# Kernel tuning notes

Measured on AMD Instinct MI355X. Metric: run time of the kernel, lower is better.

Reference implementation:

```python
import jax, jax.numpy as jnp
import numpy as np

B, S, D = 2, 2048, 1024
H, HD = 16, 64
HIDDEN = 2730  # int(1024 * 4 * 2/3)
WINDOW = 512
EPS = 1e-6


def rmsnorm(x, w):
    return x * jax.lax.rsqrt(jnp.mean(x * x, axis=-1, keepdims=True) + EPS) * w


def rope(q, k):
    # q, k: [B, H, S, HD]; half-split rotate_half convention, base 10000
    inv_freq = 1.0 / (10000.0 ** (jnp.arange(0, HD, 2, dtype=jnp.float32) / HD))
    pos = jnp.arange(S, dtype=jnp.float32)
    freqs = pos[:, None] * inv_freq[None, :]          # [S, HD/2]
    cos = jnp.concatenate([jnp.cos(freqs)] * 2, -1)    # [S, HD]
    sin = jnp.concatenate([jnp.sin(freqs)] * 2, -1)

    def rot_half(x):
        x1, x2 = jnp.split(x, 2, axis=-1)
        return jnp.concatenate([-x2, x1], axis=-1)

    q = q * cos + rot_half(q) * sin
    k = k * cos + rot_half(k) * sin
    return q, k


def setup_inputs() -> dict:
    key = jax.random.key(0)
    ks = jax.random.split(key, 6)
    return {
        "x": jax.random.normal(ks[0], (B, S, D), jnp.float32),
        "norm1_w": jnp.ones((D,), jnp.float32),
        "norm2_w": jnp.ones((D,), jnp.float32),
        "w_qkv": jax.random.normal(ks[1], (3 * D, D), jnp.float32) * 0.02,
        "qnorm_w": jnp.ones((HD,), jnp.float32),
        "knorm_w": jnp.ones((HD,), jnp.float32),
        "w_o": jax.random.normal(ks[2], (D, D), jnp.float32) * (0.02 / 2 ** 0.5),
        "w1": jax.random.normal(ks[3], (HIDDEN, D), jnp.float32) * 0.02,
        "w3": jax.random.normal(ks[4], (HIDDEN, D), jnp.float32) * 0.02,
        "w2": jax.random.normal(ks[5], (D, HIDDEN), jnp.float32) * 0.02,
    }


def reference(x, norm1_w, norm2_w, w_qkv, qnorm_w, knorm_w, w_o, w1, w3, w2):
    h = rmsnorm(x, norm1_w)                              # [B,S,D]
    qkv = jnp.einsum("bsd,ed->bse", h, w_qkv)            # [B,S,3D]
    q, k, v = jnp.split(qkv, 3, axis=-1)

    def heads(t):  # [B,S,D] -> [B,H,S,HD]
        return t.reshape(B, S, H, HD).transpose(0, 2, 1, 3)

    q, k, v = heads(q), heads(k), heads(v)
    q = rmsnorm(q, qnorm_w)  # qk_norm over head_dim
    k = rmsnorm(k, knorm_w)
    q, k = rope(q, k)

    scale = HD ** -0.5
    scores = jnp.einsum("bhqd,bhkd->bhqk", q, k) * scale  # [B,H,S,S]
    pos = jnp.arange(S)
    row, col = pos[:, None], pos[None, :]
    masked = (col > row) | (col < row - WINDOW + 1)       # True = don't attend
    scores = jnp.where(masked[None, None], -jnp.inf, scores)
    attn = jax.nn.softmax(scores, axis=-1)
    out = jnp.einsum("bhqk,bhkd->bhqd", attn, v)          # [B,H,S,HD]
    out = out.transpose(0, 2, 1, 3).reshape(B, S, D)
    out = jnp.einsum("bsd,ed->bse", out, w_o)

    x = x + out
    h2 = rmsnorm(x, norm2_w)
    gate = jax.nn.silu(jnp.einsum("bsd,hd->bsh", h2, w1))
    up = jnp.einsum("bsd,hd->bsh", h2, w3)
    ffn = jnp.einsum("bsh,dh->bsd", gate * up, w2)
    return x + ffn
```

## Files before the change

### kernel.cpp

```cpp
#include <hip/hip_runtime.h>

typedef unsigned short u16;
typedef unsigned int   u32;
typedef __bf16 bf16x8 __attribute__((ext_vector_type(8)));
typedef __bf16 bf16x2 __attribute__((ext_vector_type(2)));
typedef float  f32x4  __attribute__((ext_vector_type(4)));
typedef float  f32x2  __attribute__((ext_vector_type(2)));

#define DEV static __device__ __forceinline__
#define NEG_INF (-__builtin_inff())

DEV u16 f2bf(float f) {
  u32 u = __builtin_bit_cast(u32, f);
  u += 0x7fffu + ((u >> 16) & 1u);
  return (u16)(u >> 16);
}

DEV float bf2f(u16 v) {
  u32 u = (u32)v << 16;
  return __builtin_bit_cast(float, u);
}

DEV u32 packbf(float a, float b) {
  f32x2 v = {a, b};
  bf16x2 r = __builtin_convertvector(v, bf16x2);
  return __builtin_bit_cast(u32, r);
}

typedef __attribute__((address_space(1))) void gvoid_t;
typedef __attribute__((address_space(3))) void svoid_t;

DEV void async16(const void* g, void* l) {
  __builtin_amdgcn_global_load_lds((gvoid_t*)g, (svoid_t*)l, 16, 0, 0);
}

DEV f32x4 mfma_bf16(bf16x8 a, bf16x8 b, f32x4 c) {
  return __builtin_amdgcn_mfma_f32_16x16x32_bf16(a, b, c, 0, 0, 0);
}

#define SBAR() __builtin_amdgcn_sched_barrier(0)
#define BARRIER() do { SBAR(); __builtin_amdgcn_s_barrier(); SBAR(); } while (0)
#define LGK0() do { asm volatile("s_waitcnt lgkmcnt(0)" ::: "memory"); SBAR(); } while (0)
#define VMC(n) do { asm volatile("s_waitcnt vmcnt(" #n ")" ::: "memory"); SBAR(); } while (0)

__global__ void cvt_bf16_k(const float* __restrict__ s, u16* __restrict__ d, int n4) {
  int i = blockIdx.x * blockDim.x + threadIdx.x;
  if (i >= n4) return;
  float4 v = ((const float4*)s)[i];
  ((ushort4*)d)[i] = make_ushort4(f2bf(v.x), f2bf(v.y), f2bf(v.z), f2bf(v.w));
}

__global__ void w13_prep_k(const float* __restrict__ w1, const float* __restrict__ w3,
                           u16* __restrict__ d, int n4) {
  int i = blockIdx.x * blockDim.x + threadIdx.x;
  if (i >= n4) return;
  int e = i * 4;
  int r = e >> 10;
  int c = e & 1023;
  int blk = r >> 4, j = r & 15;
  int srow = (blk >> 1) * 16 + j;
  ushort4 o = make_ushort4(0, 0, 0, 0);
  if (srow < 2730) {
    const float* src = (blk & 1) ? w3 : w1;
    float4 v = *(const float4*)&src[(size_t)srow * 1024 + c];
    o = make_ushort4(f2bf(v.x), f2bf(v.y), f2bf(v.z), f2bf(v.w));
  }
  ((ushort4*)d)[i] = o;
}

__global__ void pad_cols_k(const float* __restrict__ s, u16* __restrict__ d,
                           int Cs, int Cd, int n4) {
  int i = blockIdx.x * blockDim.x + threadIdx.x;
  if (i >= n4) return;
  int e = i * 4;
  int r = e / Cd;
  int c = e - r * Cd;
  u16 o[4];
#pragma unroll
  for (int j = 0; j < 4; ++j) {
    int cc = c + j;
    o[j] = (cc < Cs) ? f2bf(s[(size_t)r * Cs + cc]) : (u16)0;
  }
  ((ushort4*)d)[i] = make_ushort4(o[0], o[1], o[2], o[3]);
}

__global__ void rmsnorm_cvt_k(const float* __restrict__ in, const float* __restrict__ w,
                              u16* __restrict__ out) {
  __shared__ float red[4];
  int row = blockIdx.x;
  int t = threadIdx.x;
  const float4 v = ((const float4*)(in + (size_t)row * 1024))[t];
  float ss = v.x * v.x + v.y * v.y + v.z * v.z + v.w * v.w;
#pragma unroll
  for (int off = 1; off < 64; off <<= 1) ss += __shfl_xor(ss, off);
  if ((t & 63) == 0) red[t >> 6] = ss;
  __syncthreads();
  float tot = red[0] + red[1] + red[2] + red[3];
  float rs = rsqrtf(tot * (1.0f / 1024.0f) + 1e-6f);
  const float4 wv = ((const float4*)w)[t];
  ((ushort4*)(out + (size_t)row * 1024))[t] =
      make_ushort4(f2bf(v.x * rs * wv.x), f2bf(v.y * rs * wv.y),
                   f2bf(v.z * rs * wv.z), f2bf(v.w * rs * wv.w));
}

__global__ void qk_post_k(const u16* __restrict__ qkv, const float* __restrict__ qw,
                          const float* __restrict__ kw, u16* __restrict__ Qb,
                          u16* __restrict__ Kb) {
  int g = blockIdx.x * 4 + (threadIdx.x >> 6);
  int d = threadIdx.x & 63;
  int b = g >> 15;
  int r = g & 32767;
  int s = r >> 4;
  int h = r & 15;
  size_t base = ((size_t)(b * 2048 + s)) * 3072 + h * 64 + d;
  float qv = bf2f(qkv[base]);
  float kv = bf2f(qkv[base + 1024]);
  float q2 = qv * qv, k2 = kv * kv;
#pragma unroll
  for (int off = 1; off < 64; off <<= 1) {
    q2 += __shfl_xor(q2, off);
    k2 += __shfl_xor(k2, off);
  }
  float qn = qv * rsqrtf(q2 * (1.0f / 64.0f) + 1e-6f) * qw[d];
  float kn = kv * rsqrtf(k2 * (1.0f / 64.0f) + 1e-6f) * kw[d];
  int j = d & 31;
  float invf = __expf((float)j * -0.28782313662425572f);
  float ang = (float)s * invf;
  float sn, cs;
  sincosf(ang, &sn, &cs);
  float pq = __shfl_xor(qn, 32);
  float pk = __shfl_xor(kn, 32);
  float qo = (d < 32) ? (qn * cs - pq * sn) : (qn * cs + pq * sn);
  float ko = (d < 32) ? (kn * cs - pk * sn) : (kn * cs + pk * sn);
  size_t ob = ((size_t)((b * 16 + h) * 2048 + s)) * 64 + d;
  Qb[ob] = f2bf(qo);
  Kb[ob] = f2bf(ko);
}

__global__ void vtrans_k(const u16* __restrict__ qkv, u16* __restrict__ VT) {
  __shared__ u16 tile[64][65];
  int bh = blockIdx.y;
  int b = bh >> 4, h = bh & 15;
  int s0 = blockIdx.x * 64;
  int t = threadIdx.x;
  int tx = t & 63, ty = t >> 6;
#pragma unroll
  for (int p = 0; p < 16; ++p) {
    int sl = p * 4 + ty;
    tile[sl][tx] = qkv[((size_t)(b * 2048 + s0 + sl)) * 3072 + 2048 + h * 64 + tx];
  }
  __syncthreads();
#pragma unroll
  for (int p = 0; p < 16; ++p) {
    int dl = p * 4 + ty;
    VT[((size_t)(bh * 64 + dl)) * 2048 + s0 + tx] = tile[tx][dl];
  }
}

template <int EPI>
__global__ __launch_bounds__(256, 1) void gemm128p(
    const u16* __restrict__ A, const u16* __restrict__ B0,
    const float* __restrict__ res, void* __restrict__ outp, int M, int N, int K, int NT) {
  __shared__ u16 S[49152];
  const int tid = threadIdx.x;
  const int lane = tid & 63;
  const int wv = tid >> 6;
  const int wr = wv >> 1;
  const int wc = wv & 1;
  const int c16 = lane & 15, g4 = lane >> 4;

  const int gx = gridDim.x;
  const int nwg = gx * gridDim.y;
  const int lin = blockIdx.x + gx * blockIdx.y;
  const int swz = (lin & 7) * (nwg >> 3) + (lin >> 3);
  const int bm = (swz / gx) * 128;
  const int bn = (swz % gx) * 128;

  const int strow = tid >> 3;
  const int stcs = ((tid & 7) ^ (strow & 7)) * 8;
  const u16* Ap = A + (size_t)(bm + strow) * K + stcs;
  const u16* Bp = B0 + (size_t)(bn + strow) * K + stcs;
  const int wvb = wv * 512;

#define STG(bufi, t) do { const size_t _o = (size_t)(t) * 64; _Pragma("unroll") \
    for (int s = 0; s < 4; ++s) { \
      async16(Ap + _o + (size_t)s * 32 * K, &S[(bufi) * 16384 + s * 2048 + wvb]); \
      async16(Bp + _o + (size_t)s * 32 * K, &S[(bufi) * 16384 + 8192 + s * 2048 + wvb]); \
    } } while (0)

  f32x4 acc[4][4] = {};
  const int xk0 = (g4 ^ (c16 & 7)) * 8;
  const int xk1 = ((4 + g4) ^ (c16 & 7)) * 8;
  const int arb = (wr * 64 + c16) * 64;
  const int brb = 8192 + (wc * 64 + c16) * 64;

  STG(0, 0);
  STG(1, 1);
  VMC(8); BARRIER();

  int cur = 0;
  for (int kt = 0; kt < NT; ++kt) {
    int n2 = cur + 2; if (n2 >= 3) n2 -= 3;
    if (kt + 2 < NT) {
      if (n2 == 0) STG(0, kt + 2);
      else if (n2 == 1) STG(1, kt + 2);
      else STG(2, kt + 2);
    }
    bf16x8 a[4][2], b[4][2];
    const int cb = cur * 16384;
#pragma unroll
    for (int mf = 0; mf < 4; ++mf) {
      a[mf][0] = *(const bf16x8*)&S[cb + arb + mf * 1024 + xk0];
      a[mf][1] = *(const bf16x8*)&S[cb + arb + mf * 1024 + xk1];
    }
#pragma unroll
    for (int nf = 0; nf < 4; ++nf) {
      b[nf][0] = *(const bf16x8*)&S[cb + brb + nf * 1024 + xk0];
      b[nf][1] = *(const bf16x8*)&S[cb + brb + nf * 1024 + xk1];
    }
    LGK0();
    __builtin_amdgcn_s_setprio(1);
#pragma unroll
    for (int ks = 0; ks < 2; ++ks)
#pragma unroll
      for (int mf = 0; mf < 4; ++mf)
#pragma unroll
        for (int nf = 0; nf < 4; ++nf)
          acc[mf][nf] = mfma_bf16(a[mf][ks], b[nf][ks], acc[mf][nf]);
    __builtin_amdgcn_s_setprio(0);
    if (kt + 2 < NT) { VMC(8); } else { VMC(0); }
    BARRIER();
    cur = cur + 1; if (cur >= 3) cur = 0;
  }

#pragma unroll
  for (int mf = 0; mf < 4; ++mf)
#pragma unroll
    for (int nf = 0; nf < 4; ++nf) {
      int row = bm + wr * 64 + mf * 16 + g4 * 4;
      int col = bn + wc * 64 + nf * 16 + c16;
#pragma unroll
      for (int r = 0; r < 4; ++r) {
        size_t idx = (size_t)(row + r) * (size_t)N + col;
        if constexpr (EPI == 1) {
          ((float*)outp)[idx] = res[idx] + acc[mf][nf][r];
        } else {
          ((u16*)outp)[idx] = f2bf(acc[mf][nf][r]);
        }
      }
    }
#undef STG
}

template <int QM, int QN>
DEV void mmq(f32x4 (&acc)[8][4], const bf16x8 (&a)[4][2], const bf16x8 (&b)[2][2]) {
#pragma unroll
  for (int mf = 0; mf < 4; ++mf)
#pragma unroll
    for (int nf = 0; nf < 2; ++nf) {
      acc[QM * 4 + mf][QN * 2 + nf] = mfma_bf16(a[mf][0], b[nf][0], acc[QM * 4 + mf][QN * 2 + nf]);
      acc[QM * 4 + mf][QN * 2 + nf] = mfma_bf16(a[mf][1], b[nf][1], acc[QM * 4 + mf][QN * 2 + nf]);
    }
}

template <int EPI>
__global__ __launch_bounds__(512, 2) void gemm256(
    const u16* __restrict__ A, const u16* __restrict__ B0,
    void* __restrict__ outp, int M, int N, int K, int NT) {
  __shared__ u16 S[65536];
  const int tid = threadIdx.x;
  const int lane = tid & 63;
  const int wv = tid >> 6;
  const int wr = wv >> 2;
  const int wc = wv & 3;
  const int c16 = lane & 15, g4 = lane >> 4;

  int gx = gridDim.x;
  int nwg = gx * gridDim.y;
  int lin = blockIdx.x + gx * blockIdx.y;
  int swz = ((nwg & 7) == 0) ? ((lin & 7) * (nwg >> 3) + (lin >> 3)) : lin;
  const int bm = (swz / gx) * 256;
  const int bn = (swz % gx) * 256;

  const int sr = tid >> 2;
  const int sc2s = ((tid & 3) * 16) ^ (((sr >> 3) & 1) << 5);
  const int scol = sc2s >> 1;
  const u16* Asrc = A + (size_t)(bm + sr) * K + scol;
  const u16* Bsrc = B0 + (size_t)(bn + sr) * K + scol;
  const int ldst = wv * 512;

#define STA(buf, h, t) do { \
    const u16* _g = Asrc + (size_t)(h) * 128 * K + (t) * 64; \
    async16(_g,      &S[(buf) * 16384 + (h) * 8192 + ldst]); \
    async16(_g + 32, &S[(buf) * 16384 + (h) * 8192 + 4096 + ldst]); } while (0)
#define STB(buf, h, t) do { \
    const u16* _g = Bsrc + (size_t)(h) * 128 * K + (t) * 64; \
    async16(_g,      &S[32768 + (buf) * 16384 + (h) * 8192 + ldst]); \
    async16(_g + 32, &S[32768 + (buf) * 16384 + (h) * 8192 + 4096 + ldst]); } while (0)

  const int xr = (g4 * 8) ^ (((c16 >> 3) & 1) << 4);
  const int raOff = c16 * 32 + xr;
  const int abase0 = wr * 8192;
  const int bbase0 = 32768 + (wc >> 1) * 8192 + (wc & 1) * 2048;

#define LDA(buf, qm) do { _Pragma("unroll") \
    for (int mf = 0; mf < 4; ++mf) { \
      int _ro = (buf) * 16384 + abase0 + ((qm) * 64 + mf * 16) * 32 + raOff; \
      a[mf][0] = *(const bf16x8*)&S[_ro]; \
      a[mf][1] = *(const bf16x8*)&S[_ro + 4096]; } } while (0)
#define LDB(buf, qn, bq) do { _Pragma("unroll") \
    for (int nf = 0; nf < 2; ++nf) { \
      int _ro = (buf) * 16384 + bbase0 + ((qn) * 2 + nf) * 512 + raOff; \
      bq[nf][0] = *(const bf16x8*)&S[_ro]; \
      bq[nf][1] = *(const bf16x8*)&S[_ro + 4096]; } } while (0)

  f32x4 acc[8][4] = {};
  bf16x8 a[4][2], bq0[2][2], bq1[2][2];

  STB(0, 0, 0); STA(0, 0, 0); STB(0, 1, 0); STA(0, 1, 0);
  STB(1, 0, 1); STA(1, 0, 1);
  VMC(4); BARRIER();

  for (int kt = 0; kt < NT; ++kt) {
    const int buf = kt & 1, ob = buf ^ 1;
    const int t1 = (kt + 1 < NT) ? kt + 1 : NT - 1;
    const int t2 = (kt + 2 < NT) ? kt + 2 : NT - 1;
    LDA(buf, 0); LDB(buf, 0, bq0);
    STB(ob, 1, t1);
    BARRIER(); LGK0();
    __builtin_amdgcn_s_setprio(1); mmq<0, 0>(acc, a, bq0); __builtin_amdgcn_s_setprio(0);
    BARRIER();
    LDB(buf, 1, bq1);
    STA(ob, 1, t1);
    BARRIER(); LGK0();
    __builtin_amdgcn_s_setprio(1); mmq<0, 1>(acc, a, bq1); __builtin_amdgcn_s_setprio(0);
    BARRIER();
    LDA(buf, 1);
    STB(buf, 0, t2);
    BARRIER(); LGK0();
    __builtin_amdgcn_s_setprio(1); mmq<1, 0>(acc, a, bq0); __builtin_amdgcn_s_setprio(0);
    BARRIER();
    STA(buf, 0, t2);
    BARRIER();
    __builtin_amdgcn_s_setprio(1); mmq<1, 1>(acc, a, bq1); __builtin_amdgcn_s_setprio(0);
    VMC(4); BARRIER();
  }
  asm volatile("s_waitcnt vmcnt(0)" ::: "memory");

#pragma unroll
  for (int mf = 0; mf < 8; ++mf) {
    int row0 = bm + wr * 128 + mf * 16 + g4 * 4;
    if constexpr (EPI == 0) {
#pragma unroll
      for (int nf = 0; nf < 4; ++nf) {
        int col = bn + wc * 64 + nf * 16 + c16;
#pragma unroll
        for (int r = 0; r < 4; ++r)
          ((float*)outp)[(size_t)(row0 + r) * N + col] = acc[mf][nf][r];
      }
    } else {
      const int NH = N >> 1;
#pragma unroll
      for (int p = 0; p < 2; ++p) {
        int hid = ((bn + wc * 64) >> 1) + p * 16 + c16;
#pragma unroll
        for (int r = 0; r < 4; ++r) {
          float gg = acc[mf][2 * p][r];
          float uu = acc[mf][2 * p + 1][r];
          ((u16*)outp)[(size_t)(row0 + r) * NH + hid] = f2bf(gg * uu / (1.0f + __expf(-gg)));
        }
      }
    }
  }
#undef STA
#undef STB
#undef LDA
#undef LDB
}

__global__ __launch_bounds__(256, 4) void attn_k(const u16* __restrict__ Q,
                                                 const u16* __restrict__ Kb,
                                                 const u16* __restrict__ VT,
                                                 u16* __restrict__ O) {
  __shared__ u16 KT[2 * 2048];
  __shared__ u16 VTl[2 * 2048];
  __shared__ float bsm[4][16];
  __shared__ u16 Plds[4][16 * 40];
  const int tid = threadIdx.x;
  const int lane = tid & 63;
  const int wv = tid >> 6;
  const int bh = blockIdx.y;
  const int q0b = blockIdx.x * 64;
  const int q0 = q0b + wv * 16;
  const int c16 = lane & 15;
  const int hi = lane >> 4;
  const u16* Qp = Q + ((size_t)bh * 2048 + q0) * 64;

  const bf16x8 qf0 = *(const bf16x8*)&Qp[c16 * 64 + hi * 8];
  const bf16x8 qf1 = *(const bf16x8*)&Qp[c16 * 64 + 32 + hi * 8];

  const int krow = tid >> 3;
  const int kcs = ((tid & 7) ^ (krow & 7)) * 8;
  const u16* Ksrc = Kb + (size_t)bh * 131072 + (size_t)krow * 64 + kcs;
  const int vrow = tid >> 2;
  const int vcs = ((tid & 3) ^ ((vrow >> 1) & 3)) * 8;
  const u16* Vsrc = VT + (size_t)bh * 131072 + (size_t)vrow * 2048 + vcs;
  const int wvb = wv * 512;

  f32x4 o[4] = {};
  float m = -30.0f;
  float psum = 0.0f;
  const float SCL = 0.125f * 1.4426950408889634f;
  int startb = q0b - 511;
  if (startb < 0) startb = 0;
  startb &= ~31;
  const int kgend = q0b + 32;
  u16* Pw = Plds[wv];
  float* bw = bsm[wv];

  const int xh0 = (hi ^ (c16 & 7)) * 8;
  const int xh4 = ((4 + hi) ^ (c16 & 7)) * 8;
  const int xv = (hi ^ ((c16 >> 1) & 3)) * 8;

  async16(Ksrc + (size_t)startb * 64, &KT[wvb]);
  async16(Vsrc + startb, &VTl[wvb]);

  int buf = 0;
  for (int kg = startb; kg <= kgend; kg += 32) {
    if (kg + 32 <= kgend) {
      async16(Ksrc + (size_t)(kg + 32) * 64, &KT[(buf ^ 1) * 2048 + wvb]);
      async16(Vsrc + (kg + 32), &VTl[(buf ^ 1) * 2048 + wvb]);
      VMC(2);
    } else {
      VMC(0);
    }
    BARRIER();
    if (kg <= q0 + 15 && kg >= q0 - 542) {
      const int kb = buf * 2048 + c16 * 64;
      bf16x8 k00 = *(const bf16x8*)&KT[kb + xh0];
      bf16x8 k01 = *(const bf16x8*)&KT[kb + xh4];
      bf16x8 k10 = *(const bf16x8*)&KT[kb + 1024 + xh0];
      bf16x8 k11 = *(const bf16x8*)&KT[kb + 1024 + xh4];
      bf16x8 vf[4];
#pragma unroll
      for (int n = 0; n < 4; ++n)
        vf[n] = *(const bf16x8*)&VTl[buf * 2048 + (n * 16 + c16) * 32 + xv];
      LGK0();

      f32x4 slo = {0.f, 0.f, 0.f, 0.f}, shi2 = {0.f, 0.f, 0.f, 0.f};
      __builtin_amdgcn_s_setprio(1);
      slo = mfma_bf16(k00, qf0, slo);
      slo = mfma_bf16(k01, qf1, slo);
      shi2 = mfma_bf16(k10, qf0, shi2);
      shi2 = mfma_bf16(k11, qf1, shi2);
      __builtin_amdgcn_s_setprio(0);

      float sc[8];
#pragma unroll
      for (int r = 0; r < 4; ++r) {
        sc[r] = slo[r] * SCL;
        sc[4 + r] = shi2[r] * SCL;
      }
      const bool inter = (kg + 31 <= q0) && (kg >= q0 - 496);
      if (!inter) {
        const int row = q0 + c16;
#pragma unroll
        for (int r = 0; r < 4; ++r) {
          int col = kg + hi * 4 + r;
          if (!(col <= row && col > row - 512)) sc[r] = -1e30f;
          int col2 = col + 16;
          if (!(col2 <= row && col2 > row - 512)) sc[4 + r] = -1e30f;
        }
      }
      float tmax = fmaxf(fmaxf(fmaxf(sc[0], sc[1]), fmaxf(sc[2], sc[3])),
                         fmaxf(fmaxf(sc[4], sc[5]), fmaxf(sc[6], sc[7])));
      tmax = fmaxf(tmax, __shfl_xor(tmax, 16));
      tmax = fmaxf(tmax, __shfl_xor(tmax, 32));
      if (__any(tmax > m + 8.0f)) {
        float mn = fmaxf(m, tmax);
        float corr = exp2f(m - mn);
        m = mn;
        psum *= corr;
        bw[c16] = corr;
        __builtin_amdgcn_wave_barrier();
        float cr[4];
#pragma unroll
        for (int r = 0; r < 4; ++r) cr[r] = bw[hi * 4 + r];
        __builtin_amdgcn_wave_barrier();
#pragma unroll
        for (int n = 0; n < 4; ++n)
#pragma unroll
          for (int r = 0; r < 4; ++r) o[n][r] *= cr[r];
      }
      float p[8];
#pragma unroll
      for (int i = 0; i < 8; ++i) p[i] = exp2f(sc[i] - m);
      psum += ((p[0] + p[1]) + (p[2] + p[3])) + ((p[4] + p[5]) + (p[6] + p[7]));

      uint2 wlo, whi2;
      wlo.x = packbf(p[0], p[1]);
      wlo.y = packbf(p[2], p[3]);
      whi2.x = packbf(p[4], p[5]);
      whi2.y = packbf(p[6], p[7]);
      *(uint2*)&Pw[c16 * 40 + hi * 4] = wlo;
      *(uint2*)&Pw[c16 * 40 + 16 + hi * 4] = whi2;
      __builtin_amdgcn_wave_barrier();
      bf16x8 pa = *(const bf16x8*)&Pw[c16 * 40 + hi * 8];
      __builtin_amdgcn_wave_barrier();
      __builtin_amdgcn_s_setprio(1);
#pragma unroll
      for (int n = 0; n < 4; ++n) o[n] = mfma_bf16(pa, vf[n], o[n]);
      __builtin_amdgcn_s_setprio(0);
    }
    BARRIER();
    buf ^= 1;
  }

  psum += __shfl_xor(psum, 16);
  psum += __shfl_xor(psum, 32);
  bw[c16] = psum;
  __builtin_amdgcn_wave_barrier();
  const int b = bh >> 4, h = bh & 15;
#pragma unroll
  for (int r = 0; r < 4; ++r) {
    float inv = 1.0f / bw[hi * 4 + r];
    int row = q0 + hi * 4 + r;
#pragma unroll
    for (int n = 0; n < 4; ++n)
      O[((size_t)(b * 2048 + row)) * 1024 + h * 64 + n * 16 + c16] = f2bf(o[n][r] * inv);
  }
}

extern "C" void kernel_launch(void* const* d_in, const int* in_sizes, int n_in,
                              void* d_out, int out_size, void* d_ws, size_t ws_size,
                              hipStream_t stream) {
  const float* x    = (const float*)d_in[0];
  const float* n1w  = (const float*)d_in[1];
  const float* n2w  = (const float*)d_in[2];
  const float* wqkv = (const float*)d_in[3];
  const float* qnw  = (const float*)d_in[4];
  const float* knw  = (const float*)d_in[5];
  const float* wo   = (const float*)d_in[6];
  const float* w1   = (const float*)d_in[7];
  const float* w3   = (const float*)d_in[8];
  const float* w2   = (const float*)d_in[9];
  float* out = (float*)d_out;
  char* ws = (char*)d_ws;

  u16*   wqkv_b = (u16*)(ws + 0);
  u16*   wo_b   = (u16*)(ws + 6291456);
  u16*   w13i   = (u16*)(ws + 8388608);
  u16*   w2p    = (u16*)(ws + 19922944);
  u16*   h_b    = (u16*)(ws + 25690112);
  u16*   qkv_b  = (u16*)(ws + 34078720);
  u16*   act_b  = (u16*)(ws + 34078720);
  u16*   Qb     = (u16*)(ws + 84410368);
  u16*   Kb     = (u16*)(ws + 92798976);
  u16*   VTb    = (u16*)(ws + 101187584);
  float* x2f    = (float*)(ws + 109576192);
  u16*   attn_b = h_b;
  u16*   h2_b   = Qb;

  cvt_bf16_k<<<3072, 256, 0, stream>>>(wqkv, wqkv_b, 786432);
  cvt_bf16_k<<<1024, 256, 0, stream>>>(wo, wo_b, 262144);
  w13_prep_k<<<5632, 256, 0, stream>>>(w1, w3, w13i, 1441792);
  pad_cols_k<<<2816, 256, 0, stream>>>(w2, w2p, 2730, 2816, 720896);

  rmsnorm_cvt_k<<<4096, 256, 0, stream>>>(x, n1w, h_b);
  gemm128p<2><<<dim3(24, 32), 256, 0, stream>>>(h_b, wqkv_b, nullptr, qkv_b,
                                                4096, 3072, 1024, 16);
  qk_post_k<<<16384, 256, 0, stream>>>(qkv_b, qnw, knw, Qb, Kb);
  vtrans_k<<<dim3(32, 32), 256, 0, stream>>>(qkv_b, VTb);
  attn_k<<<dim3(32, 32), 256, 0, stream>>>(Qb, Kb, VTb, attn_b);
  gemm128p<1><<<dim3(8, 32), 256, 0, stream>>>(attn_b, wo_b, x, x2f, 4096, 1024, 1024, 16);
  rmsnorm_cvt_k<<<4096, 256, 0, stream>>>(x2f, n2w, h2_b);
  gemm256<3><<<dim3(22, 16), 512, 0, stream>>>(h2_b, w13i, act_b, 4096, 5632, 1024, 16);
  gemm128p<1><<<dim3(8, 32), 256, 0, stream>>>(act_b, w2p, x2f, out, 4096, 1024, 2816, 44);
}
```

Measured before the change: 240.1 us.

## Add 256x192-tile pipelined GEMM kernel for the QKV projection

```diff
diff --git a/kernel.cpp b/kernel.cpp
--- a/kernel.cpp
+++ b/kernel.cpp
@@ -250,6 +250,126 @@
       }
     }
 #undef STG
+}
+
+__global__ __launch_bounds__(512, 1) void gemm192(
+    const u16* __restrict__ A, const u16* __restrict__ B0,
+    u16* __restrict__ outp, int N, int K, int NT) {
+  __shared__ u16 SA[32768];
+  __shared__ u16 SB[24576];
+  const int tid = threadIdx.x;
+  const int lane = tid & 63;
+  const int wv = tid >> 6;
+  const int wr = wv >> 2;
+  const int wc = wv & 3;
+  const int c16 = lane & 15, g4 = lane >> 4;
+
+  const int gx = gridDim.x;
+  const int nwg = gx * gridDim.y;
+  const int lin = blockIdx.x + gx * blockIdx.y;
+  const int swz = (lin & 7) * (nwg >> 3) + (lin >> 3);
+  const int bm = (swz / gx) * 256;
+  const int bn = (swz % gx) * 192;
+
+  const int sr = tid >> 2;
+  const int sc2s = ((tid & 3) * 16) ^ (((sr >> 3) & 1) << 5);
+  const int scol = sc2s >> 1;
+  const u16* Asrc = A + (size_t)(bm + sr) * K + scol;
+  const int ldst = wv * 512;
+  const int brow = tid >> 3;
+  const int bgr = (tid & 7) ^ (brow & 7);
+  const u16* Bsrc = B0 + (size_t)(bn + brow) * K + bgr * 8;
+  const int bldst = wv * 512;
+
+#define STA_(buf, h, t) do { \
+    const u16* _g = Asrc + (size_t)(h) * 128 * K + (t) * 64; \
+    async16(_g,      &SA[(buf) * 16384 + (h) * 8192 + ldst]); \
+    async16(_g + 32, &SA[(buf) * 16384 + (h) * 8192 + 4096 + ldst]); } while (0)
+#define STB_(buf, p, t) do { \
+    async16(Bsrc + (size_t)(p) * 64 * K + (t) * 64, \
+            &SB[(buf) * 12288 + (p) * 4096 + bldst]); } while (0)
+
+  const int xr = (g4 * 8) ^ (((c16 >> 3) & 1) << 4);
+  const int raOff = c16 * 32 + xr;
+  const int abase0 = wr * 8192;
+  const int brow0 = wc * 48 + c16;
+  const int bsw = c16 & 7;
+
+#define LDA_(buf, qm) do { _Pragma("unroll") \
+    for (int mf = 0; mf < 4; ++mf) { \
+      int _ro = (buf) * 16384 + abase0 + ((qm) * 64 + mf * 16) * 32 + raOff; \
+      a[mf][0] = *(const bf16x8*)&SA[_ro]; \
+      a[mf][1] = *(const bf16x8*)&SA[_ro + 4096]; } } while (0)
+#define LDB01_(buf) do { _Pragma("unroll") \
+    for (int nf = 0; nf < 2; ++nf) { \
+      int _r = (buf) * 12288 + (brow0 + nf * 16) * 64; \
+      bq01[nf][0] = *(const bf16x8*)&SB[_r + ((g4) ^ bsw) * 8]; \
+      bq01[nf][1] = *(const bf16x8*)&SB[_r + ((4 + g4) ^ bsw) * 8]; } } while (0)
+#define LDB2_(buf) do { \
+      int _r = (buf) * 12288 + (brow0 + 32) * 64; \
+      bq2[0] = *(const bf16x8*)&SB[_r + ((g4) ^ bsw) * 8]; \
+      bq2[1] = *(const bf16x8*)&SB[_r + ((4 + g4) ^ bsw) * 8]; } while (0)
+#define MM16(qm) do { _Pragma("unroll") \
+    for (int mf = 0; mf < 4; ++mf) _Pragma("unroll") \
+      for (int nf = 0; nf < 2; ++nf) { \
+        acc[(qm) * 4 + mf][nf] = mfma_bf16(a[mf][0], bq01[nf][0], acc[(qm) * 4 + mf][nf]); \
+        acc[(qm) * 4 + mf][nf] = mfma_bf16(a[mf][1], bq01[nf][1], acc[(qm) * 4 + mf][nf]); } } while (0)
+#define MM8(qm) do { _Pragma("unroll") \
+    for (int mf = 0; mf < 4; ++mf) { \
+      acc[(qm) * 4 + mf][2] = mfma_bf16(a[mf][0], bq2[0], acc[(qm) * 4 + mf][2]); \
+      acc[(qm) * 4 + mf][2] = mfma_bf16(a[mf][1], bq2[1], acc[(qm) * 4 + mf][2]); } } while (0)
+
+  f32x4 acc[8][3] = {};
+  bf16x8 a[4][2], bq01[2][2], bq2[2];
+
+  STB_(0, 0, 0); STB_(0, 1, 0); STB_(0, 2, 0); STA_(0, 0, 0); STA_(0, 1, 0);
+  STB_(1, 0, 1); STB_(1, 1, 1); STA_(1, 0, 1);
+  VMC(4); BARRIER();
+
+  for (int kt = 0; kt < NT; ++kt) {
+    const int buf = kt & 1, ob = buf ^ 1;
+    const int t1 = (kt + 1 < NT) ? kt + 1 : NT - 1;
+    const int t2 = (kt + 2 < NT) ? kt + 2 : NT - 1;
+    LDA_(buf, 0); LDB01_(buf);
+    STB_(ob, 2, t1);
+    BARRIER(); LGK0();
+    __builtin_amdgcn_s_setprio(1); MM16(0); __builtin_amdgcn_s_setprio(0);
+    BARRIER();
+    LDB2_(buf);
+    STA_(ob, 1, t1);
+    BARRIER(); LGK0();
+    __builtin_amdgcn_s_setprio(1); MM8(0); __builtin_amdgcn_s_setprio(0);
+    BARRIER();
+    LDA_(buf, 1);
+    STB_(buf, 0, t2); STB_(buf, 1, t2);
+    BARRIER(); LGK0();
+    __builtin_amdgcn_s_setprio(1); MM16(1); __builtin_amdgcn_s_setprio(0);
+    BARRIER();
+    STA_(buf, 0, t2);
+    BARRIER();
+    __builtin_amdgcn_s_setprio(1); MM8(1); __builtin_amdgcn_s_setprio(0);
+    VMC(4); BARRIER();
+  }
+  asm volatile("s_waitcnt vmcnt(0)" ::: "memory");
+
+#pragma unroll
+  for (int mf = 0; mf < 8; ++mf) {
+    int row0 = bm + wr * 128 + mf * 16 + g4 * 4;
+#pragma unroll
+    for (int nf = 0; nf < 3; ++nf) {
+      int col = bn + wc * 48 + nf * 16 + c16;
+#pragma unroll
+      for (int r = 0; r < 4; ++r)
+        outp[(size_t)(row0 + r) * N + col] = f2bf(acc[mf][nf][r]);
+    }
+  }
+#undef STA_
+#undef STB_
+#undef LDA_
+#undef LDB01_
+#undef LDB2_
+#undef MM16
+#undef MM8
 }
 
 template <int QM, int QN>
@@ -567,8 +687,7 @@
   pad_cols_k<<<2816, 256, 0, stream>>>(w2, w2p, 2730, 2816, 720896);
 
   rmsnorm_cvt_k<<<4096, 256, 0, stream>>>(x, n1w, h_b);
-  gemm128p<2><<<dim3(24, 32), 256, 0, stream>>>(h_b, wqkv_b, nullptr, qkv_b,
-                                                4096, 3072, 1024, 16);
+  gemm192<<<dim3(16, 16), 512, 0, stream>>>(h_b, wqkv_b, qkv_b, 3072, 1024, 16);
   qk_post_k<<<16384, 256, 0, stream>>>(qkv_b, qnw, knw, Qb, Kb);
   vtrans_k<<<dim3(32, 32), 256, 0, stream>>>(qkv_b, VTb);
   attn_k<<<dim3(32, 32), 256, 0, stream>>>(Qb, Kb, VTb, attn_b);
```

New measurement: 232.5 us. 3.2% less time.

## Run 128x128 GEMM with 8 waves and replace gemm256 with it

Applied to the files above, without the earlier changes.

```diff
diff --git a/kernel.cpp b/kernel.cpp
--- a/kernel.cpp
+++ b/kernel.cpp
@@ -158,7 +158,7 @@
 }
 
 template <int EPI>
-__global__ __launch_bounds__(256, 1) void gemm128p(
+__global__ __launch_bounds__(512, 1) void gemm128p(
     const u16* __restrict__ A, const u16* __restrict__ B0,
     const float* __restrict__ res, void* __restrict__ outp, int M, int N, int K, int NT) {
   __shared__ u16 S[49152];
@@ -182,21 +182,22 @@
   const u16* Bp = B0 + (size_t)(bn + strow) * K + stcs;
   const int wvb = wv * 512;
 
-#define STG(bufi, t) do { const size_t _o = (size_t)(t) * 64; _Pragma("unroll") \
-    for (int s = 0; s < 4; ++s) { \
-      async16(Ap + _o + (size_t)s * 32 * K, &S[(bufi) * 16384 + s * 2048 + wvb]); \
-      async16(Bp + _o + (size_t)s * 32 * K, &S[(bufi) * 16384 + 8192 + s * 2048 + wvb]); \
-    } } while (0)
-
-  f32x4 acc[4][4] = {};
+#define STG(bufi, t) do { const size_t _o = (size_t)(t) * 64; \
+      async16(Ap + _o,                    &S[(bufi) * 16384 +         wvb]); \
+      async16(Ap + _o + (size_t)64 * K,   &S[(bufi) * 16384 +  4096 + wvb]); \
+      async16(Bp + _o,                    &S[(bufi) * 16384 +  8192 + wvb]); \
+      async16(Bp + _o + (size_t)64 * K,   &S[(bufi) * 16384 + 12288 + wvb]); \
+    } while (0)
+
+  f32x4 acc[2][4] = {};
   const int xk0 = (g4 ^ (c16 & 7)) * 8;
   const int xk1 = ((4 + g4) ^ (c16 & 7)) * 8;
-  const int arb = (wr * 64 + c16) * 64;
+  const int arb = (wr * 32 + c16) * 64;
   const int brb = 8192 + (wc * 64 + c16) * 64;
 
   STG(0, 0);
   STG(1, 1);
-  VMC(8); BARRIER();
+  VMC(4); BARRIER();
 
   int cur = 0;
   for (int kt = 0; kt < NT; ++kt) {
@@ -206,10 +207,10 @@
       else if (n2 == 1) STG(1, kt + 2);
       else STG(2, kt + 2);
     }
-    bf16x8 a[4][2], b[4][2];
+    bf16x8 a[2][2], b[4][2];
     const int cb = cur * 16384;
 #pragma unroll
-    for (int mf = 0; mf < 4; ++mf) {
+    for (int mf = 0; mf < 2; ++mf) {
       a[mf][0] = *(const bf16x8*)&S[cb + arb + mf * 1024 + xk0];
       a[mf][1] = *(const bf16x8*)&S[cb + arb + mf * 1024 + xk1];
     }
@@ -223,143 +224,21 @@
 #pragma unroll
     for (int ks = 0; ks < 2; ++ks)
 #pragma unroll
-      for (int mf = 0; mf < 4; ++mf)
+      for (int mf = 0; mf < 2; ++mf)
 #pragma unroll
         for (int nf = 0; nf < 4; ++nf)
           acc[mf][nf] = mfma_bf16(a[mf][ks], b[nf][ks], acc[mf][nf]);
     __builtin_amdgcn_s_setprio(0);
-    if (kt + 2 < NT) { VMC(8); } else { VMC(0); }
+    if (kt + 2 < NT) { VMC(4); } else { VMC(0); }
     BARRIER();
     cur = cur + 1; if (cur >= 3) cur = 0;
   }
 
-#pragma unroll
-  for (int mf = 0; mf < 4; ++mf)
-#pragma unroll
-    for (int nf = 0; nf < 4; ++nf) {
-      int row = bm + wr * 64 + mf * 16 + g4 * 4;
-      int col = bn + wc * 64 + nf * 16 + c16;
-#pragma unroll
-      for (int r = 0; r < 4; ++r) {
-        size_t idx = (size_t)(row + r) * (size_t)N + col;
-        if constexpr (EPI == 1) {
-          ((float*)outp)[idx] = res[idx] + acc[mf][nf][r];
-        } else {
-          ((u16*)outp)[idx] = f2bf(acc[mf][nf][r]);
-        }
-      }
-    }
-#undef STG
-}
-
-template <int QM, int QN>
-DEV void mmq(f32x4 (&acc)[8][4], const bf16x8 (&a)[4][2], const bf16x8 (&b)[2][2]) {
-#pragma unroll
-  for (int mf = 0; mf < 4; ++mf)
-#pragma unroll
-    for (int nf = 0; nf < 2; ++nf) {
-      acc[QM * 4 + mf][QN * 2 + nf] = mfma_bf16(a[mf][0], b[nf][0], acc[QM * 4 + mf][QN * 2 + nf]);
-      acc[QM * 4 + mf][QN * 2 + nf] = mfma_bf16(a[mf][1], b[nf][1], acc[QM * 4 + mf][QN * 2 + nf]);
-    }
-}
-
-template <int EPI>
-__global__ __launch_bounds__(512, 2) void gemm256(
-    const u16* __restrict__ A, const u16* __restrict__ B0,
-    void* __restrict__ outp, int M, int N, int K, int NT) {
-  __shared__ u16 S[65536];
-  const int tid = threadIdx.x;
-  const int lane = tid & 63;
-  const int wv = tid >> 6;
-  const int wr = wv >> 2;
-  const int wc = wv & 3;
-  const int c16 = lane & 15, g4 = lane >> 4;
-
-  int gx = gridDim.x;
-  int nwg = gx * gridDim.y;
-  int lin = blockIdx.x + gx * blockIdx.y;
-  int swz = ((nwg & 7) == 0) ? ((lin & 7) * (nwg >> 3) + (lin >> 3)) : lin;
-  const int bm = (swz / gx) * 256;
-  const int bn = (swz % gx) * 256;
-
-  const int sr = tid >> 2;
-  const int sc2s = ((tid & 3) * 16) ^ (((sr >> 3) & 1) << 5);
-  const int scol = sc2s >> 1;
-  const u16* Asrc = A + (size_t)(bm + sr) * K + scol;
-  const u16* Bsrc = B0 + (size_t)(bn + sr) * K + scol;
-  const int ldst = wv * 512;
-
-#define STA(buf, h, t) do { \
-    const u16* _g = Asrc + (size_t)(h) * 128 * K + (t) * 64; \
-    async16(_g,      &S[(buf) * 16384 + (h) * 8192 + ldst]); \
-    async16(_g + 32, &S[(buf) * 16384 + (h) * 8192 + 4096 + ldst]); } while (0)
-#define STB(buf, h, t) do { \
-    const u16* _g = Bsrc + (size_t)(h) * 128 * K + (t) * 64; \
-    async16(_g,      &S[32768 + (buf) * 16384 + (h) * 8192 + ldst]); \
-    async16(_g + 32, &S[32768 + (buf) * 16384 + (h) * 8192 + 4096 + ldst]); } while (0)
-
-  const int xr = (g4 * 8) ^ (((c16 >> 3) & 1) << 4);
-  const int raOff = c16 * 32 + xr;
-  const int abase0 = wr * 8192;
-  const int bbase0 = 32768 + (wc >> 1) * 8192 + (wc & 1) * 2048;
-
-#define LDA(buf, qm) do { _Pragma("unroll") \
-    for (int mf = 0; mf < 4; ++mf) { \
-      int _ro = (buf) * 16384 + abase0 + ((qm) * 64 + mf * 16) * 32 + raOff; \
-      a[mf][0] = *(const bf16x8*)&S[_ro]; \
-      a[mf][1] = *(const bf16x8*)&S[_ro + 4096]; } } while (0)
-#define LDB(buf, qn, bq) do { _Pragma("unroll") \
-    for (int nf = 0; nf < 2; ++nf) { \
-      int _ro = (buf) * 16384 + bbase0 + ((qn) * 2 + nf) * 512 + raOff; \
-      bq[nf][0] = *(const bf16x8*)&S[_ro]; \
-      bq[nf][1] = *(const bf16x8*)&S[_ro + 4096]; } } while (0)
-
-  f32x4 acc[8][4] = {};
-  bf16x8 a[4][2], bq0[2][2], bq1[2][2];
-
-  STB(0, 0, 0); STA(0, 0, 0); STB(0, 1, 0); STA(0, 1, 0);
-  STB(1, 0, 1); STA(1, 0, 1);
-  VMC(4); BARRIER();
-
-  for (int kt = 0; kt < NT; ++kt) {
-    const int buf = kt & 1, ob = buf ^ 1;
-    const int t1 = (kt + 1 < NT) ? kt + 1 : NT - 1;
-    const int t2 = (kt + 2 < NT) ? kt + 2 : NT - 1;
-    LDA(buf, 0); LDB(buf, 0, bq0);
-    STB(ob, 1, t1);
-    BARRIER(); LGK0();
-    __builtin_amdgcn_s_setprio(1); mmq<0, 0>(acc, a, bq0); __builtin_amdgcn_s_setprio(0);
-    BARRIER();
-    LDB(buf, 1, bq1);
-    STA(ob, 1, t1);
-    BARRIER(); LGK0();
-    __builtin_amdgcn_s_setprio(1); mmq<0, 1>(acc, a, bq1); __builtin_amdgcn_s_setprio(0);
-    BARRIER();
-    LDA(buf, 1);
-    STB(buf, 0, t2);
-    BARRIER(); LGK0();
-    __builtin_amdgcn_s_setprio(1); mmq<1, 0>(acc, a, bq0); __builtin_amdgcn_s_setprio(0);
-    BARRIER();
-    STA(buf, 0, t2);
-    BARRIER();
-    __builtin_amdgcn_s_setprio(1); mmq<1, 1>(acc, a, bq1); __builtin_amdgcn_s_setprio(0);
-    VMC(4); BARRIER();
-  }
-  asm volatile("s_waitcnt vmcnt(0)" ::: "memory");
-
-#pragma unroll
-  for (int mf = 0; mf < 8; ++mf) {
-    int row0 = bm + wr * 128 + mf * 16 + g4 * 4;
-    if constexpr (EPI == 0) {
-#pragma unroll
-      for (int nf = 0; nf < 4; ++nf) {
-        int col = bn + wc * 64 + nf * 16 + c16;
-#pragma unroll
-        for (int r = 0; r < 4; ++r)
-          ((float*)outp)[(size_t)(row0 + r) * N + col] = acc[mf][nf][r];
-      }
-    } else {
-      const int NH = N >> 1;
+  if constexpr (EPI == 3) {
+    const int NH = N >> 1;
+#pragma unroll
+    for (int mf = 0; mf < 2; ++mf) {
+      int row0 = bm + wr * 32 + mf * 16 + g4 * 4;
 #pragma unroll
       for (int p = 0; p < 2; ++p) {
         int hid = ((bn + wc * 64) >> 1) + p * 16 + c16;
@@ -371,11 +250,25 @@
         }
       }
     }
-  }
-#undef STA
-#undef STB
-#undef LDA
-#undef LDB
+  } else {
+#pragma unroll
+    for (int mf = 0; mf < 2; ++mf)
+#pragma unroll
+      for (int nf = 0; nf < 4; ++nf) {
+        int row = bm + wr * 32 + mf * 16 + g4 * 4;
+        int col = bn + wc * 64 + nf * 16 + c16;
+#pragma unroll
+        for (int r = 0; r < 4; ++r) {
+          size_t idx = (size_t)(row + r) * (size_t)N + col;
+          if constexpr (EPI == 1) {
+            ((float*)outp)[idx] = res[idx] + acc[mf][nf][r];
+          } else {
+            ((u16*)outp)[idx] = f2bf(acc[mf][nf][r]);
+          }
+        }
+      }
+  }
+#undef STG
 }
 
 __global__ __launch_bounds__(256, 4) void attn_k(const u16* __restrict__ Q,
@@ -567,13 +460,14 @@
   pad_cols_k<<<2816, 256, 0, stream>>>(w2, w2p, 2730, 2816, 720896);
 
   rmsnorm_cvt_k<<<4096, 256, 0, stream>>>(x, n1w, h_b);
-  gemm128p<2><<<dim3(24, 32), 256, 0, stream>>>(h_b, wqkv_b, nullptr, qkv_b,
+  gemm128p<2><<<dim3(24, 32), 512, 0, stream>>>(h_b, wqkv_b, nullptr, qkv_b,
                                                 4096, 3072, 1024, 16);
   qk_post_k<<<16384, 256, 0, stream>>>(qkv_b, qnw, knw, Qb, Kb);
   vtrans_k<<<dim3(32, 32), 256, 0, stream>>>(qkv_b, VTb);
   attn_k<<<dim3(32, 32), 256, 0, stream>>>(Qb, Kb, VTb, attn_b);
-  gemm128p<1><<<dim3(8, 32), 256, 0, stream>>>(attn_b, wo_b, x, x2f, 4096, 1024, 1024, 16);
+  gemm128p<1><<<dim3(8, 32), 512, 0, stream>>>(attn_b, wo_b, x, x2f, 4096, 1024, 1024, 16);
   rmsnorm_cvt_k<<<4096, 256, 0, stream>>>(x2f, n2w, h2_b);
-  gemm256<3><<<dim3(22, 16), 512, 0, stream>>>(h2_b, w13i, act_b, 4096, 5632, 1024, 16);
-  gemm128p<1><<<dim3(8, 32), 256, 0, stream>>>(act_b, w2p, x2f, out, 4096, 1024, 2816, 44);
-}
+  gemm128p<3><<<dim3(44, 32), 512, 0, stream>>>(h2_b, w13i, nullptr, act_b,
+                                                4096, 5632, 1024, 16);
+  gemm128p<1><<<dim3(8, 32), 512, 0, stream>>>(act_b, w2p, x2f, out, 4096, 1024, 2816, 44);
+}
```

Result: slower. 245.2 us (+2.1%).
